# Kernel optimization log

Measured on AMD Instinct MI355X. Metric: run time of the kernel, lower is better.

The kernel has to match this reference:

```python
import jax, jax.numpy as jnp
import numpy as np

N, E, D_IN, D_OUT = 100000, 1600000, 64, 64


def setup_inputs() -> dict:
    key = jax.random.key(0)
    k0, k1, k2, k3 = jax.random.split(key, 4)
    x = jax.random.normal(k0, (N, D_IN), dtype=jnp.float32)
    edge_index = jax.random.randint(k1, (2, E), 0, N)  # [2, E] (src, dst)
    W = jax.random.normal(k2, (D_IN, D_OUT), dtype=jnp.float32) / np.sqrt(D_IN).astype(np.float32)
    b = jnp.zeros((D_OUT,), dtype=jnp.float32)
    causal_attention = jax.random.normal(k3, (D_OUT, D_OUT), dtype=jnp.float32)
    return {"x": x, "edge_index": edge_index, "W": W, "b": b,
            "causal_attention": causal_attention, "L": 1}


def gcn_conv(x, edge_index, W, b):
    # PyG GCNConv: x' = D^{-1/2} (A + I) D^{-1/2} (x W) + b
    n = x.shape[0]
    xw = x @ W  # [N, D_OUT]
    loops = jnp.arange(n)
    src = jnp.concatenate([edge_index[0], loops])  # [E+N]
    dst = jnp.concatenate([edge_index[1], loops])
    deg = jax.ops.segment_sum(jnp.ones_like(src, dtype=xw.dtype), dst, num_segments=n)
    dinv = jnp.where(deg > 0, jax.lax.rsqrt(deg), 0.0)
    norm = dinv[src] * dinv[dst]  # [E+N]
    agg = jax.ops.segment_sum(norm[:, None] * xw[src], dst, num_segments=n)  # [N, D_OUT]
    return agg + b


def reference(x, edge_index, W, b, causal_attention, L):
    x_conv = gcn_conv(x, edge_index, W, b)
    causal_weights = jax.nn.softmax(causal_attention, axis=1)  # row softmax
    return x_conv @ causal_weights  # [N, D_OUT]
```

## Files before the change

### kernel.cpp

```cpp
#include <hip/hip_runtime.h>
#include <hip/hip_bf16.h>


#define D 64
#define BSHIFT 6
#define BNODES 64
#define ARENA_CAP 1728
#define BIN_TILE 8192

__device__ __forceinline__ unsigned short f2bf(float f) {
    union { float f; unsigned int u; } c;
    c.f = f;
    unsigned int u = c.u;
    u += 0x7fffu + ((u >> 16) & 1u);
    return (unsigned short)(u >> 16);
}
__device__ __forceinline__ float bflo(unsigned int u) {
    union { unsigned int u; float f; } c;
    c.u = u << 16;
    return c.f;
}
__device__ __forceinline__ float bfhi(unsigned int u) {
    union { unsigned int u; float f; } c;
    c.u = u & 0xffff0000u;
    return c.f;
}

__global__ __launch_bounds__(256) void prep_kernel(const float* __restrict__ W,
                                                   const float* __restrict__ b,
                                                   const float* __restrict__ A,
                                                   float* __restrict__ M,
                                                   float* __restrict__ bs,
                                                   int* __restrict__ cursor, int nbuck) {
    __shared__ float S[D * D];
    int t = threadIdx.x;
    int gidx = blockIdx.x * 256 + t;
    if (gidx < nbuck) cursor[gidx] = gidx * ARENA_CAP;
    int wv = t >> 6, lane = t & 63;
#pragma unroll 4
    for (int rr = 0; rr < 16; rr++) {
        int r = wv * 16 + rr;
        float a = A[r * D + lane];
        float m = a;
        for (int off = 32; off; off >>= 1) m = fmaxf(m, __shfl_xor(m, off));
        float p = __expf(a - m);
        float ssum = p;
        for (int off = 32; off; off >>= 1) ssum += __shfl_xor(ssum, off);
        S[r * D + lane] = p / ssum;
    }
    __syncthreads();
    int k = blockIdx.x * 4 + wv;
    float acc = 0.f;
    for (int d2 = 0; d2 < D; d2++) acc += W[k * D + d2] * S[d2 * D + lane];
    M[k * D + lane] = acc;
    if (blockIdx.x == 0 && t < D) {
        float a2 = 0.f;
        for (int d2 = 0; d2 < D; d2++) a2 += b[d2] * S[d2 * D + t];
        bs[t] = a2;
    }
}

__global__ __launch_bounds__(512) void bin_kernel(const int* __restrict__ src,
                                                  const int* __restrict__ dst,
                                                  int* __restrict__ cursor,
                                                  int* __restrict__ binned, int E) {
    __shared__ int h[2048];
    int t = threadIdx.x;
    for (int i = t; i < 2048; i += 512) h[i] = 0;
    __syncthreads();
    int base = blockIdx.x * BIN_TILE;
    int pv[16], bk[16], rv[16];
#pragma unroll
    for (int k = 0; k < 16; k++) {
        int e = base + k * 512 + t;
        if (e < E) {
            int s = src[e], d = dst[e];
            bk[k] = (d >> BSHIFT) & 2047;
            pv[k] = (s << BSHIFT) | (d & (BNODES - 1));
            rv[k] = atomicAdd(&h[bk[k]], 1);
        }
    }
    __syncthreads();
    for (int b2 = t; b2 < 2048; b2 += 512) {
        int c = h[b2];
        if (c) h[b2] = atomicAdd(&cursor[b2], c);
    }
    __syncthreads();
#pragma unroll
    for (int k = 0; k < 16; k++) {
        int e = base + k * 512 + t;
        if (e < E) binned[h[bk[k]] + rv[k]] = pv[k];
    }
}

__global__ __launch_bounds__(256) void sort_kernel(int* __restrict__ binned,
                                                   const int* __restrict__ cursor,
                                                   int* __restrict__ rowstart,
                                                   int* __restrict__ rowend,
                                                   float* __restrict__ dinv,
                                                   int N) {
    __shared__ int buf[ARENA_CAP];
    __shared__ int h[BNODES];
    __shared__ int cur[BNODES];
    int t = threadIdx.x;
    int b = blockIdx.x;
    int s = b * ARENA_CAP;
    int cnt = cursor[b] - s;
    if (cnt > ARENA_CAP) cnt = ARENA_CAP;
    if (t < BNODES) h[t] = 0;
    __syncthreads();
    for (int i = t; i < cnt; i += 256) {
        int p = binned[s + i];
        buf[i] = p;
        atomicAdd(&h[p & (BNODES - 1)], 1);
    }
    __syncthreads();
    if (t < BNODES) {
        int v = h[t];
        int sc = v;
#pragma unroll
        for (int off = 1; off < BNODES; off <<= 1) {
            int u = __shfl_up(sc, off);
            if (t >= off) sc += u;
        }
        cur[t] = sc - v;
        int node = (b << BSHIFT) + t;
        if (node < N) {
            rowstart[node] = s + sc - v;
            rowend[node] = s + sc;
            dinv[node] = rsqrtf((float)(v + 1));
        }
    }
    __syncthreads();
    for (int i = t; i < cnt; i += 256) {
        int p = buf[i];
        int pos = atomicAdd(&cur[p & (BNODES - 1)], 1);
        binned[s + pos] = (int)((unsigned)p >> BSHIFT);
    }
}

__device__ __forceinline__ void fma4(float4& a, float xv, const float4& m) {
    a.x += xv * m.x; a.y += xv * m.y; a.z += xv * m.z; a.w += xv * m.w;
}
__global__ __launch_bounds__(256) void zmat_kernel(const float* __restrict__ x,
                                                   const float* __restrict__ M,
                                                   const float* __restrict__ dinv,
                                                   unsigned short* __restrict__ zbf,
                                                   int N) {
    __shared__ float Ms[D * D];
    __shared__ float xs[64][D + 4];
    int t = threadIdx.x;
    int row0 = blockIdx.x << 6;
    for (int i = t; i < (D * D) / 4; i += 256)
        ((float4*)Ms)[i] = ((const float4*)M)[i];
    for (int w = t; w < 1024; w += 256) {
        int r = w >> 4, c4 = (w & 15) << 2;
        int row = row0 + r;
        float4 v = make_float4(0.f, 0.f, 0.f, 0.f);
        if (row < N) v = *(const float4*)&x[(size_t)row * D + c4];
        *(float4*)&xs[r][c4] = v;
    }
    __syncthreads();
    int cg = t & 15, rg = t >> 4;
    int r0 = rg << 2, c0 = cg << 2;
    float4 a0 = make_float4(0.f, 0.f, 0.f, 0.f);
    float4 a1 = a0, a2 = a0, a3 = a0;
#pragma unroll 4
    for (int k = 0; k < D; k += 4) {
        float4 x0 = *(const float4*)&xs[r0 + 0][k];
        float4 x1 = *(const float4*)&xs[r0 + 1][k];
        float4 x2 = *(const float4*)&xs[r0 + 2][k];
        float4 x3 = *(const float4*)&xs[r0 + 3][k];
        float4 m0 = *(const float4*)&Ms[(k + 0) * D + c0];
        float4 m1 = *(const float4*)&Ms[(k + 1) * D + c0];
        float4 m2 = *(const float4*)&Ms[(k + 2) * D + c0];
        float4 m3 = *(const float4*)&Ms[(k + 3) * D + c0];
        fma4(a0, x0.x, m0); fma4(a0, x0.y, m1); fma4(a0, x0.z, m2); fma4(a0, x0.w, m3);
        fma4(a1, x1.x, m0); fma4(a1, x1.y, m1); fma4(a1, x1.z, m2); fma4(a1, x1.w, m3);
        fma4(a2, x2.x, m0); fma4(a2, x2.y, m1); fma4(a2, x2.z, m2); fma4(a2, x2.w, m3);
        fma4(a3, x3.x, m0); fma4(a3, x3.y, m1); fma4(a3, x3.z, m2); fma4(a3, x3.w, m3);
    }
    int rowb = row0 + r0;
    if (rowb < N) {
        float4 dv4 = *(const float4*)&dinv[rowb];
        ushort4 s0, s1, s2, s3;
        s0.x = f2bf(dv4.x * a0.x); s0.y = f2bf(dv4.x * a0.y);
        s0.z = f2bf(dv4.x * a0.z); s0.w = f2bf(dv4.x * a0.w);
        s1.x = f2bf(dv4.y * a1.x); s1.y = f2bf(dv4.y * a1.y);
        s1.z = f2bf(dv4.y * a1.z); s1.w = f2bf(dv4.y * a1.w);
        s2.x = f2bf(dv4.z * a2.x); s2.y = f2bf(dv4.z * a2.y);
        s2.z = f2bf(dv4.z * a2.z); s2.w = f2bf(dv4.z * a2.w);
        s3.x = f2bf(dv4.w * a3.x); s3.y = f2bf(dv4.w * a3.y);
        s3.z = f2bf(dv4.w * a3.z); s3.w = f2bf(dv4.w * a3.w);
        *(ushort4*)&zbf[(size_t)(rowb + 0) * D + c0] = s0;
        *(ushort4*)&zbf[(size_t)(rowb + 1) * D + c0] = s1;
        *(ushort4*)&zbf[(size_t)(rowb + 2) * D + c0] = s2;
        *(ushort4*)&zbf[(size_t)(rowb + 3) * D + c0] = s3;
    }
}

__global__ __launch_bounds__(256) void gather_kernel(const unsigned short* __restrict__ zbf,
                                                     const int* __restrict__ csr,
                                                     const int* __restrict__ rowstart,
                                                     const int* __restrict__ rowend,
                                                     const float* __restrict__ dinv,
                                                     const float* __restrict__ bs,
                                                     float* __restrict__ out, int n) {
    int node = blockIdx.x * 4 + (threadIdx.x >> 6);
    if (node >= n) return;
    int lane = threadIdx.x & 63;
    int g = lane >> 5;
    int c = lane & 31;
    int start = rowstart[node];
    int end = rowend[node];
    float a0 = 0.f, a1 = 0.f, a2 = 0.f, a3 = 0.f;
    int e = start;
    while (e < end) {
        int cnt = min(end - e, 64);
        int sreg = (lane < cnt) ? csr[e + lane] : 0;
        int k = 0;
        for (; k + 7 < cnt; k += 8) {
            int p0 = __shfl(sreg, k + g);
            int p1 = __shfl(sreg, k + 2 + g);
            int p2 = __shfl(sreg, k + 4 + g);
            int p3 = __shfl(sreg, k + 6 + g);
            unsigned u0 = *(const unsigned*)&zbf[(size_t)p0 * D + 2 * c];
            unsigned u1 = *(const unsigned*)&zbf[(size_t)p1 * D + 2 * c];
            unsigned u2 = *(const unsigned*)&zbf[(size_t)p2 * D + 2 * c];
            unsigned u3 = *(const unsigned*)&zbf[(size_t)p3 * D + 2 * c];
            a0 += bflo(u0); a1 += bfhi(u0);
            a2 += bflo(u1); a3 += bfhi(u1);
            a0 += bflo(u2); a1 += bfhi(u2);
            a2 += bflo(u3); a3 += bfhi(u3);
        }
        for (; k + 1 < cnt; k += 2) {
            int p = __shfl(sreg, k + g);
            unsigned u = *(const unsigned*)&zbf[(size_t)p * D + 2 * c];
            a0 += bflo(u); a1 += bfhi(u);
        }
        if (k < cnt) {
            int p = __shfl(sreg, k);
            unsigned u = *(const unsigned*)&zbf[(size_t)p * D + 2 * c];
            if (g == 0) { a0 += bflo(u); a1 += bfhi(u); }
        }
        e += cnt;
    }
    a0 += a2; a1 += a3;
    a0 += __shfl_xor(a0, 32);
    a1 += __shfl_xor(a1, 32);
    if (lane < 32) {
        unsigned uz = *(const unsigned*)&zbf[(size_t)node * D + 2 * c];
        float2 bb = ((const float2*)bs)[c];
        float di = dinv[node];
        float2 o;
        o.x = di * (a0 + bflo(uz)) + bb.x;
        o.y = di * (a1 + bfhi(uz)) + bb.y;
        ((float2*)&out[(size_t)node * D])[c] = o;
    }
}

extern "C" void kernel_launch(void* const* d_in, const int* in_sizes, int n_in,
                              void* d_out, int out_size, void* d_ws, size_t ws_size,
                              hipStream_t stream) {
    const float* x = (const float*)d_in[0];
    const int* ei = (const int*)d_in[1];
    const float* W = (const float*)d_in[2];
    const float* b = (const float*)d_in[3];
    const float* A = (const float*)d_in[4];

    const int N = in_sizes[0] / D;
    const int E = in_sizes[1] / 2;
    const int* src = ei;
    const int* dst = ei + E;
    const int NBUCK = (N + BNODES - 1) >> BSHIFT;

    char* ws = (char*)d_ws;
    size_t off = 0;
    auto alloc = [&](size_t bytes) -> char* {
        char* p = ws + off;
        off = (off + bytes + 255) & ~(size_t)255;
        return p;
    };
    int* cursor = (int*)alloc((size_t)NBUCK * 4);
    float* dinv = (float*)alloc((size_t)N * 4);
    float* M = (float*)alloc((size_t)D * D * 4);
    float* bs = (float*)alloc((size_t)D * 4);
    int* binned = (int*)alloc((size_t)NBUCK * ARENA_CAP * 4);
    int* rowstart = (int*)alloc((size_t)N * 4);
    int* rowend = (int*)alloc((size_t)N * 4);
    unsigned short* zbf = (unsigned short*)alloc((size_t)N * D * 2);
    (void)ws_size;

    prep_kernel<<<16, 256, 0, stream>>>(W, b, A, M, bs, cursor, NBUCK);
    bin_kernel<<<(E + BIN_TILE - 1) / BIN_TILE, 512, 0, stream>>>(src, dst, cursor, binned, E);
    sort_kernel<<<NBUCK, 256, 0, stream>>>(binned, cursor, rowstart, rowend, dinv, N);
    zmat_kernel<<<(N + 63) >> 6, 256, 0, stream>>>(x, M, dinv, zbf, N);
    gather_kernel<<<(N + 3) / 4, 256, 0, stream>>>(zbf, binned, rowstart, rowend, dinv, bs, (float*)d_out, N);
}
```

Measured before the change: 181.5 us.

## Make gather kernel persistent with software-prefetched row metadata and wider loads

Converts the per-node gather kernel into a grid-stride persistent kernel with a fixed grid. While node A is processed, it prefetches the CSR row bounds, first neighbor chunk, self feature and dinv for the next nodes. It also switches from 2-element to 4-element bf16 loads, with 4 neighbors in flight per wave and an extra shuffle-reduction stage. The goal is to hide the latency of dependent metadata loads and cut instruction count per gathered row, at the cost of more registers and a fixed grid size that may not suit every occupancy level.

```diff
diff --git a/kernel.cpp b/kernel.cpp
--- a/kernel.cpp
+++ b/kernel.cpp
@@ -206,56 +206,100 @@
                                                      const float* __restrict__ dinv,
                                                      const float* __restrict__ bs,
                                                      float* __restrict__ out, int n) {
-    int node = blockIdx.x * 4 + (threadIdx.x >> 6);
-    if (node >= n) return;
+    int wid = blockIdx.x * 4 + (threadIdx.x >> 6);
     int lane = threadIdx.x & 63;
-    int g = lane >> 5;
-    int c = lane & 31;
-    int start = rowstart[node];
-    int end = rowend[node];
-    float a0 = 0.f, a1 = 0.f, a2 = 0.f, a3 = 0.f;
-    int e = start;
-    while (e < end) {
-        int cnt = min(end - e, 64);
-        int sreg = (lane < cnt) ? csr[e + lane] : 0;
-        int k = 0;
-        for (; k + 7 < cnt; k += 8) {
-            int p0 = __shfl(sreg, k + g);
-            int p1 = __shfl(sreg, k + 2 + g);
-            int p2 = __shfl(sreg, k + 4 + g);
-            int p3 = __shfl(sreg, k + 6 + g);
-            unsigned u0 = *(const unsigned*)&zbf[(size_t)p0 * D + 2 * c];
-            unsigned u1 = *(const unsigned*)&zbf[(size_t)p1 * D + 2 * c];
-            unsigned u2 = *(const unsigned*)&zbf[(size_t)p2 * D + 2 * c];
-            unsigned u3 = *(const unsigned*)&zbf[(size_t)p3 * D + 2 * c];
-            a0 += bflo(u0); a1 += bfhi(u0);
-            a2 += bflo(u1); a3 += bfhi(u1);
-            a0 += bflo(u2); a1 += bfhi(u2);
-            a2 += bflo(u3); a3 += bfhi(u3);
-        }
-        for (; k + 1 < cnt; k += 2) {
-            int p = __shfl(sreg, k + g);
-            unsigned u = *(const unsigned*)&zbf[(size_t)p * D + 2 * c];
-            a0 += bflo(u); a1 += bfhi(u);
-        }
-        if (k < cnt) {
-            int p = __shfl(sreg, k);
-            unsigned u = *(const unsigned*)&zbf[(size_t)p * D + 2 * c];
-            if (g == 0) { a0 += bflo(u); a1 += bfhi(u); }
-        }
-        e += cnt;
-    }
-    a0 += a2; a1 += a3;
-    a0 += __shfl_xor(a0, 32);
-    a1 += __shfl_xor(a1, 32);
-    if (lane < 32) {
-        unsigned uz = *(const unsigned*)&zbf[(size_t)node * D + 2 * c];
-        float2 bb = ((const float2*)bs)[c];
-        float di = dinv[node];
-        float2 o;
-        o.x = di * (a0 + bflo(uz)) + bb.x;
-        o.y = di * (a1 + bfhi(uz)) + bb.y;
-        ((float2*)&out[(size_t)node * D])[c] = o;
+    int qg = lane >> 4;
+    int c4 = lane & 15;
+    int stride = gridDim.x << 2;
+    float4 bb = ((const float4*)bs)[c4];
+
+    int nodeA = wid;
+    int sA = 0, eA = 0;
+    if (nodeA < n) { sA = rowstart[nodeA]; eA = rowend[nodeA]; }
+    int nodeB = nodeA + stride;
+    int sB = 0, eB = 0;
+    if (nodeB < n) { sB = rowstart[nodeB]; eB = rowend[nodeB]; }
+    int sregA = 0; uint2 uzA = make_uint2(0u, 0u); float diA = 0.f;
+    if (nodeA < n) {
+        int c0 = min(eA - sA, 64);
+        if (lane < c0) sregA = csr[sA + lane];
+        uzA = *(const uint2*)&zbf[(size_t)nodeA * D + 4 * c4];
+        diA = dinv[nodeA];
+    }
+
+    while (nodeA < n) {
+        int sregB = 0; uint2 uzB = make_uint2(0u, 0u); float diB = 0.f;
+        if (nodeB < n) {
+            int c0 = min(eB - sB, 64);
+            if (lane < c0) sregB = csr[sB + lane];
+            uzB = *(const uint2*)&zbf[(size_t)nodeB * D + 4 * c4];
+            diB = dinv[nodeB];
+        }
+        int nodeC = nodeB + stride;
+        int sC = 0, eC = 0;
+        if (nodeC < n) { sC = rowstart[nodeC]; eC = rowend[nodeC]; }
+
+        float a0 = 0.f, a1 = 0.f, a2 = 0.f, a3 = 0.f;
+        int e = sA;
+        bool first = true;
+        while (e < eA) {
+            int cnt = min(eA - e, 64);
+            int sreg = sregA;
+            if (!first) sreg = (lane < cnt) ? csr[e + lane] : 0;
+            first = false;
+            int k = 0;
+            for (; k + 15 < cnt; k += 16) {
+                int p0 = __shfl(sreg, k + qg);
+                int p1 = __shfl(sreg, k + 4 + qg);
+                int p2 = __shfl(sreg, k + 8 + qg);
+                int p3 = __shfl(sreg, k + 12 + qg);
+                uint2 u0 = *(const uint2*)&zbf[(size_t)p0 * D + 4 * c4];
+                uint2 u1 = *(const uint2*)&zbf[(size_t)p1 * D + 4 * c4];
+                uint2 u2 = *(const uint2*)&zbf[(size_t)p2 * D + 4 * c4];
+                uint2 u3 = *(const uint2*)&zbf[(size_t)p3 * D + 4 * c4];
+                a0 += bflo(u0.x); a1 += bfhi(u0.x); a2 += bflo(u0.y); a3 += bfhi(u0.y);
+                a0 += bflo(u1.x); a1 += bfhi(u1.x); a2 += bflo(u1.y); a3 += bfhi(u1.y);
+                a0 += bflo(u2.x); a1 += bfhi(u2.x); a2 += bflo(u2.y); a3 += bfhi(u2.y);
+                a0 += bflo(u3.x); a1 += bfhi(u3.x); a2 += bflo(u3.y); a3 += bfhi(u3.y);
+            }
+            for (; k + 7 < cnt; k += 8) {
+                int p0 = __shfl(sreg, k + qg);
+                int p1 = __shfl(sreg, k + 4 + qg);
+                uint2 u0 = *(const uint2*)&zbf[(size_t)p0 * D + 4 * c4];
+                uint2 u1 = *(const uint2*)&zbf[(size_t)p1 * D + 4 * c4];
+                a0 += bflo(u0.x); a1 += bfhi(u0.x); a2 += bflo(u0.y); a3 += bfhi(u0.y);
+                a0 += bflo(u1.x); a1 += bfhi(u1.x); a2 += bflo(u1.y); a3 += bfhi(u1.y);
+            }
+            for (; k + 3 < cnt; k += 4) {
+                int p0 = __shfl(sreg, k + qg);
+                uint2 u0 = *(const uint2*)&zbf[(size_t)p0 * D + 4 * c4];
+                a0 += bflo(u0.x); a1 += bfhi(u0.x); a2 += bflo(u0.y); a3 += bfhi(u0.y);
+            }
+            int r = cnt - k;
+            if (r) {
+                int p0 = __shfl(sreg, k + (qg < r ? qg : 0));
+                uint2 u0 = *(const uint2*)&zbf[(size_t)p0 * D + 4 * c4];
+                if (qg < r) {
+                    a0 += bflo(u0.x); a1 += bfhi(u0.x);
+                    a2 += bflo(u0.y); a3 += bfhi(u0.y);
+                }
+            }
+            e += cnt;
+        }
+        a0 += __shfl_xor(a0, 16); a1 += __shfl_xor(a1, 16);
+        a2 += __shfl_xor(a2, 16); a3 += __shfl_xor(a3, 16);
+        a0 += __shfl_xor(a0, 32); a1 += __shfl_xor(a1, 32);
+        a2 += __shfl_xor(a2, 32); a3 += __shfl_xor(a3, 32);
+        if (lane < 16) {
+            float4 o;
+            o.x = diA * (a0 + bflo(uzA.x)) + bb.x;
+            o.y = diA * (a1 + bfhi(uzA.x)) + bb.y;
+            o.z = diA * (a2 + bflo(uzA.y)) + bb.z;
+            o.w = diA * (a3 + bfhi(uzA.y)) + bb.w;
+            *(float4*)&out[(size_t)nodeA * D + 4 * c4] = o;
+        }
+        nodeA = nodeB; sA = sB; eA = eB; sregA = sregB; uzA = uzB; diA = diB;
+        nodeB = nodeC; sB = sC; eB = eC;
     }
 }
 
@@ -295,5 +339,5 @@
     bin_kernel<<<(E + BIN_TILE - 1) / BIN_TILE, 512, 0, stream>>>(src, dst, cursor, binned, E);
     sort_kernel<<<NBUCK, 256, 0, stream>>>(binned, cursor, rowstart, rowend, dinv, N);
     zmat_kernel<<<(N + 63) >> 6, 256, 0, stream>>>(x, M, dinv, zbf, N);
-    gather_kernel<<<(N + 3) / 4, 256, 0, stream>>>(zbf, binned, rowstart, rowend, dinv, bs, (float*)d_out, N);
-}
+    gather_kernel<<<2048, 256, 0, stream>>>(zbf, binned, rowstart, rowend, dinv, bs, (float*)d_out, N);
+}
```

Result: faster. 171.8 us (-5.3%).
